# Kernel tuning notes

Hardware: AMD Instinct MI355X
Metric: run time of the kernel (lower is better)

Reference implementation:

```python
import jax, jax.numpy as jnp
import numpy as np

ALPHA = 32.0 ** 2
HEADS = 8
DIM_HEAD = 64
EPS = 1e-5


def _leaky(x):
    return jnp.where(x >= 0, x, 0.1 * x)


def _cpb_bias(fmap_size, w0, b0, w1, b1, w2, b2):
    # continuous position bias: MLP over signed-log relative coords -> [h, n, n]
    pos = jnp.arange(fmap_size)
    gi, gj = jnp.meshgrid(pos, pos, indexing='ij')
    grid = jnp.stack([gi, gj], axis=-1).reshape(-1, 2)  # [n, 2]
    rel = grid[:, None, :] - grid[None, :, :]           # [n, n, 2]
    rel = jnp.sign(rel) * jnp.log(jnp.abs(rel) + 1.0)
    h = _leaky(jnp.einsum('ijc,dc->ijd', rel.astype(jnp.float32), w0) + b0)
    h = _leaky(jnp.einsum('ijc,dc->ijd', h, w1) + b1)
    h = jnp.einsum('ijc,hc->ijh', h, w2) + b2           # [n, n, heads]
    return jnp.transpose(h, (2, 0, 1))                  # [heads, n, n]


def _stable_softmax(t, alpha=ALPHA):
    t = t / alpha
    t = t - jax.lax.stop_gradient(jnp.max(t, axis=-1, keepdims=True))
    return jax.nn.softmax(t * alpha, axis=-1)


def setup_inputs() -> dict:
    key = jax.random.key(0)
    ks = jax.random.split(key, 9)
    B, C, H, W = 8, 512, 32, 32
    inner = HEADS * DIM_HEAD
    s = 0.05
    return {
        'x': jax.random.normal(ks[0], (B, C, H, W), jnp.float32),
        'gamma': jnp.ones((1, C, 1, 1), jnp.float32),
        'w_qkv': jax.random.normal(ks[1], (inner * 3, C), jnp.float32) * s,
        'w_out': jax.random.normal(ks[2], (C, inner), jnp.float32) * s,
        'cpb_w0': jax.random.normal(ks[3], (128, 2), jnp.float32) * s,
        'cpb_b0': jax.random.normal(ks[4], (128,), jnp.float32) * s,
        'cpb_w1': jax.random.normal(ks[5], (128, 128), jnp.float32) * s,
        'cpb_b1': jax.random.normal(ks[6], (128,), jnp.float32) * s,
        'cpb_w2': jax.random.normal(ks[7], (HEADS, 128), jnp.float32) * s,
        'cpb_b2': jax.random.normal(ks[8], (HEADS,), jnp.float32) * s,
    }


def reference(x, gamma, w_qkv, w_out, cpb_w0, cpb_b0, cpb_w1, cpb_b1, cpb_w2, cpb_b2):
    B, C, H, W = x.shape
    n = H * W
    scale = DIM_HEAD ** -0.5
    residual = x

    # LayerNormChan: normalize over channel dim with biased variance
    mean = jnp.mean(x, axis=1, keepdims=True)
    var = jnp.var(x, axis=1, keepdims=True)
    xn = (x - mean) / jnp.sqrt(var + EPS) * gamma

    # 1x1 conv qkv projection as matmul over channels
    xf = xn.reshape(B, C, n)                              # [B, C, n]
    qkv = jnp.einsum('oc,bcn->bon', w_qkv, xf)            # [B, 3*inner, n]
    q, k, v = jnp.split(qkv, 3, axis=1)
    rs = lambda t: t.reshape(B, HEADS, DIM_HEAD, n)
    q, k, v = rs(q), rs(k), rs(v)

    sim = jnp.einsum('bhdi,bhdj->bhij', q, k) * scale     # [B, h, n, n]
    bias = _cpb_bias(H, cpb_w0, cpb_b0, cpb_w1, cpb_b1, cpb_w2, cpb_b2)
    sim = sim + bias[None]

    attn = _stable_softmax(sim)
    out = jnp.einsum('bhij,bhdj->bhdi', attn, v)          # [B, h, d, n]
    out = out.reshape(B, HEADS * DIM_HEAD, n)
    out = jnp.einsum('oc,bcn->bon', w_out, out).reshape(B, C, H, W)
    return out + residual
```

## Files before the change

kernel.cpp:

```cpp
#include <hip/hip_runtime.h>
#include <hip/hip_bf16.h>

#define CCH   512
#define BATCH 8
#define NPOS  1024
#define MQKV  1536
#define EPS   1e-5f
#define LOG2E 1.4426950408889634f

typedef __attribute__((ext_vector_type(4))) float f32x4;
typedef __attribute__((ext_vector_type(8))) __bf16 bf16x8;
typedef __attribute__((ext_vector_type(8))) unsigned short u16x8;
typedef __attribute__((ext_vector_type(4))) unsigned short u16x4;

__device__ inline unsigned short f2bf(float f) {
  __hip_bfloat16 h = __float2bfloat16(f);
  return __builtin_bit_cast(unsigned short, h);
}
__device__ inline float bf2f(unsigned short u) {
  return __bfloat162float(__builtin_bit_cast(__hip_bfloat16, u));
}

__device__ inline int sw(int row, int col) { return row * 64 + (col ^ ((row & 7) << 3)); }
__device__ inline int swk(int row, int col) { return row * 64 + (col ^ (((row >> 2) & 7) << 3)); }
__device__ inline int sw32(int row, int lh) {
  return row * 32 + ((lh ^ ((row ^ (row >> 2)) & 3)) << 3);
}

__device__ inline void gload16(const void* g, void* l) {
  __builtin_amdgcn_global_load_lds((const __attribute__((address_space(1))) void*)g,
                                   (__attribute__((address_space(3))) void*)l, 16, 0, 0);
}

#define CBAR(N) do {                                              \
    asm volatile("s_waitcnt vmcnt(" #N ")" ::: "memory");         \
    asm volatile("s_waitcnt lgkmcnt(0)" ::: "memory");            \
    __builtin_amdgcn_s_barrier();                                 \
  } while (0)

__global__ __launch_bounds__(256) void setup_kernel(
    const float* __restrict__ wq, const float* __restrict__ wo,
    unsigned short* __restrict__ wqb, unsigned short* __restrict__ wob,
    const float* __restrict__ x, const float* __restrict__ gamma,
    unsigned short* __restrict__ xnT,
    const float* __restrict__ table, unsigned short* __restrict__ biasP) {
  __shared__ float red[4][32][2];
  __shared__ float gsh[512];
  __shared__ unsigned short obuf[32 * 520];
  int bid = blockIdx.x, tid = threadIdx.x;

  if (bid >= 640) {
    int base = ((bid - 640) * 256 + tid) * 8;
    int h = base >> 20;
    int i = (base >> 10) & 1023;
    int j0 = base & 1023;
    int ib = i >> 5, il = i & 31;
    u16x8 outv;
    #pragma unroll
    for (int e = 0; e < 8; ++e) {
      int j = j0 + e;
      int dy = ib - (j >> 5) + 31;
      int dx = il - (j & 31) + 31;
      outv[e] = f2bf(table[h * 3969 + dy * 63 + dx]);
    }
    *(u16x8*)&biasP[base] = outv;
    return;
  }

  if (bid < 384) {
    int base = bid * 2048 + tid * 8;
    float sc = (base < 512 * CCH) ? (0.125f * LOG2E) : 1.0f;
    f32x4 v0 = *(const f32x4*)&wq[base];
    f32x4 v1 = *(const f32x4*)&wq[base + 4];
    u16x8 outv;
    #pragma unroll
    for (int e = 0; e < 4; ++e) outv[e] = f2bf(v0[e] * sc);
    #pragma unroll
    for (int e = 0; e < 4; ++e) outv[4 + e] = f2bf(v1[e] * sc);
    *(u16x8*)&wqb[base] = outv;
    if (base < CCH * CCH) {
      f32x4 w0v = *(const f32x4*)&wo[base];
      f32x4 w1v = *(const f32x4*)&wo[base + 4];
      u16x8 ov;
      #pragma unroll
      for (int e = 0; e < 4; ++e) ov[e] = f2bf(w0v[e]);
      #pragma unroll
      for (int e = 0; e < 4; ++e) ov[4 + e] = f2bf(w1v[e]);
      *(u16x8*)&wob[base] = ov;
    }
  } else {
    int blk = bid - 384;
    int b = blk >> 5, p0 = (blk & 31) * 32;
    int pl = tid & 31, wv = tid >> 6, cg = tid >> 5;
    gsh[tid] = gamma[tid];
    gsh[tid + 256] = gamma[tid + 256];
    const float* xp = x + (size_t)b * CCH * NPOS + p0 + pl;
    float vals[64];
    float s1 = 0.f, s2 = 0.f;
    #pragma unroll
    for (int j = 0; j < 64; ++j) {
      float v = xp[(size_t)(cg + 8 * j) * NPOS];
      vals[j] = v; s1 += v; s2 += v * v;
    }
    s1 += __shfl_xor(s1, 32, 64); s2 += __shfl_xor(s2, 32, 64);
    if ((tid & 63) < 32) { red[wv][pl][0] = s1; red[wv][pl][1] = s2; }
    __syncthreads();
    float t1 = 0.f, t2 = 0.f;
    #pragma unroll
    for (int w2i = 0; w2i < 4; ++w2i) { t1 += red[w2i][pl][0]; t2 += red[w2i][pl][1]; }
    float mean = t1 * (1.f / 512.f);
    float var = t2 * (1.f / 512.f) - mean * mean;
    float rstd = rsqrtf(var + EPS);
    #pragma unroll
    for (int j = 0; j < 64; ++j) {
      int c = cg + 8 * j;
      obuf[pl * 520 + c] = f2bf((vals[j] - mean) * rstd * gsh[c]);
    }
    __syncthreads();
    unsigned short* orow = xnT + ((size_t)b * NPOS + p0) * 512;
    #pragma unroll
    for (int i = 0; i < 8; ++i) {
      int c2 = tid + i * 256;
      int pp = c2 >> 6, ch = c2 & 63;
      *(u16x8*)&orow[(size_t)pp * 512 + ch * 8] = *(const u16x8*)&obuf[pp * 520 + ch * 8];
    }
  }
}

__global__ __launch_bounds__(256) void cpb_kernel(
    const float* __restrict__ w0, const float* __restrict__ b0,
    const float* __restrict__ w1, const float* __restrict__ b1,
    const float* __restrict__ w2, const float* __restrict__ b2,
    float* __restrict__ table) {
  __shared__ float w1s[128 * 129];
  __shared__ float w2s[8 * 128];
  __shared__ float sh1[2][128];
  __shared__ float sh2[2][128];
  int tid = threadIdx.x;
  #pragma unroll
  for (int i = 0; i < 64; ++i) {
    int idx = i * 256 + tid;
    w1s[(idx >> 7) * 129 + (idx & 127)] = w1[idx];
  }
  #pragma unroll
  for (int i = 0; i < 4; ++i) {
    int idx = i * 256 + tid;
    w2s[idx] = w2[idx];
  }
  int sub = tid >> 7, t = tid & 127;
  float w00 = w0[t * 2 + 0], w01 = w0[t * 2 + 1], bb0 = b0[t], bb1 = b1[t];
  int hh = t >> 4, k16 = t & 15;
  float b2h = b2[hh];
  __syncthreads();

  #pragma unroll 1
  for (int pass = 0; pass < 8; ++pass) {
    int d0 = (blockIdx.x * 8 + pass) * 2 + sub;
    bool ok = d0 < 3969;
    int d0c = ok ? d0 : 0;
    int dy = d0c / 63 - 31, dx = d0c % 63 - 31;
    float r0 = (dy > 0 ? 1.f : (dy < 0 ? -1.f : 0.f)) * logf(fabsf((float)dy) + 1.f);
    float r1 = (dx > 0 ? 1.f : (dx < 0 ? -1.f : 0.f)) * logf(fabsf((float)dx) + 1.f);
    float h0 = r0 * w00 + r1 * w01 + bb0;
    sh1[sub][t] = (h0 >= 0.f) ? h0 : 0.1f * h0;
    __syncthreads();
    float a = bb1;
    #pragma unroll 8
    for (int c = 0; c < 128; ++c) a += sh1[sub][c] * w1s[t * 129 + c];
    sh2[sub][t] = (a >= 0.f) ? a : 0.1f * a;
    __syncthreads();
    float o = 0.f;
    #pragma unroll
    for (int c = 0; c < 8; ++c) o += sh2[sub][k16 * 8 + c] * w2s[hh * 128 + k16 * 8 + c];
    #pragma unroll
    for (int mm = 1; mm < 16; mm <<= 1) o += __shfl_xor(o, mm, 64);
    if (k16 == 0 && ok) table[hh * 3969 + d0] = (o + b2h) * LOG2E;
    __syncthreads();
  }
}

__global__ __launch_bounds__(256) void gemm_qkv(const unsigned short* __restrict__ Ag,
                                                const unsigned short* __restrict__ Bg,
                                                unsigned short* __restrict__ qT,
                                                unsigned short* __restrict__ kT,
                                                unsigned short* __restrict__ vB) {
  __shared__ unsigned short smem[24576];
  int tid = threadIdx.x;
  int by = blockIdx.y;
  int m0 = by * 128, nn0 = blockIdx.x * 128;
  int wave = tid >> 6, lane = tid & 63;
  int wm = wave >> 1, wn = wave & 1;
  int l16 = lane & 15, lh = lane >> 4;
  int r4 = lane >> 2, c4 = lane & 3;
  int csw = ((c4 ^ (r4 & 3) ^ ((lane >> 4) & 3))) << 3;
  f32x4 acc[4][4];
  #pragma unroll
  for (int it = 0; it < 4; ++it)
    #pragma unroll
    for (int jt = 0; jt < 4; ++jt) acc[it][jt] = (f32x4){0.f, 0.f, 0.f, 0.f};

  #define GSTAGE(bsel, k0) do {                                                               \
    _Pragma("unroll")                                                                         \
    for (int i_ = 0; i_ < 2; ++i_) {                                                          \
      int grp_ = wave * 2 + i_;                                                               \
      int row_ = grp_ * 16 + r4;                                                              \
      gload16(&Ag[(size_t)(m0 + row_) * 512 + (k0) + csw], smem + (bsel) * 4096 + grp_ * 512);\
      gload16(&Bg[(size_t)(nn0 + row_) * 512 + (k0) + csw],                                   \
              smem + 12288 + (bsel) * 4096 + grp_ * 512);                                     \
    }                                                                                         \
  } while (0)

  GSTAGE(0, 0);
  GSTAGE(1, 32);
  asm volatile("s_waitcnt vmcnt(4)" ::: "memory");
  __builtin_amdgcn_s_barrier();
  int cur = 0;
  #pragma unroll 1
  for (int k = 0; k < 16; ++k) {
    int stg = (cur == 0) ? 2 : cur - 1;
    if (k < 14) GSTAGE(stg, (k + 2) * 32);
    const unsigned short* As = smem + cur * 4096;
    const unsigned short* Bs = smem + 12288 + cur * 4096;
    bf16x8 a[4], b[4];
    #pragma unroll
    for (int it = 0; it < 4; ++it) a[it] = *(const bf16x8*)&As[sw32(wm * 64 + it * 16 + l16, lh)];
    #pragma unroll
    for (int jt = 0; jt < 4; ++jt) b[jt] = *(const bf16x8*)&Bs[sw32(wn * 64 + jt * 16 + l16, lh)];
    __builtin_amdgcn_s_setprio(1);
    #pragma unroll
    for (int it = 0; it < 4; ++it)
      #pragma unroll
      for (int jt = 0; jt < 4; ++jt)
        acc[it][jt] = __builtin_amdgcn_mfma_f32_16x16x32_bf16(a[it], b[jt], acc[it][jt], 0, 0, 0);
    __builtin_amdgcn_s_setprio(0);
    if (k < 14) CBAR(4); else CBAR(0);
    cur = (cur == 2) ? 0 : cur + 1;
  }

  int sel = by >> 2;
  int hh0 = (by & 3) * 2;
  int bb = nn0 >> 10, p0 = nn0 & 1023;
  unsigned short* Cs = smem;
  if (sel < 2) {
    #pragma unroll
    for (int it = 0; it < 4; ++it)
      #pragma unroll
      for (int jt = 0; jt < 4; ++jt) {
        int nnl = wn * 64 + jt * 16 + l16;
        int mb = wm * 64 + it * 16 + lh * 4;
        #pragma unroll
        for (int r = 0; r < 4; ++r)
          Cs[nnl * 128 + ((mb + r) ^ ((nnl & 7) << 4))] = f2bf(acc[it][jt][r]);
      }
    __syncthreads();
    unsigned short* dst = (sel == 0) ? qT : kT;
    #pragma unroll
    for (int i = 0; i < 8; ++i) {
      int c = tid + i * 256;
      int hl = c >> 10, p = (c >> 3) & 127, ch = c & 7;
      int mb = hl * 64 + ch * 8;
      u16x8 val = *(u16x8*)&Cs[p * 128 + (mb ^ ((p & 7) << 4))];
      int bh = bb * 8 + hh0 + hl;
      *(u16x8*)&dst[((size_t)bh * 1024 + p0 + p) * 64 + ch * 8] = val;
    }
  } else {
    #pragma unroll
    for (int it = 0; it < 4; ++it)
      #pragma unroll
      for (int jt = 0; jt < 4; ++jt) {
        int nnl = wn * 64 + jt * 16 + l16;
        int mb = wm * 64 + it * 16 + lh * 4;
        #pragma unroll
        for (int r = 0; r < 4; ++r)
          Cs[(mb + r) * 128 + (nnl ^ (((mb + r) & 7) << 4))] = f2bf(acc[it][jt][r]);
      }
    __syncthreads();
    #pragma unroll
    for (int i = 0; i < 8; ++i) {
      int c = tid + i * 256;
      int mloc = c >> 4, ch = c & 15;
      u16x8 val = *(u16x8*)&Cs[mloc * 128 + ((ch * 8) ^ ((mloc & 7) << 4))];
      int d = mloc & 63, hl = mloc >> 6;
      int bh = bb * 8 + hh0 + hl;
      *(u16x8*)&vB[((size_t)bh * 64 + d) * 1024 + p0 + ch * 8] = val;
    }
  }
}

__global__ __launch_bounds__(256) void gemm_out(const unsigned short* __restrict__ Ag,
                                                const unsigned short* __restrict__ Bg,
                                                const float* __restrict__ xres,
                                                float* __restrict__ yout) {
  __shared__ unsigned short smem[18432];
  int tid = threadIdx.x;
  int m0 = blockIdx.y * 64, nn0 = blockIdx.x * 128;
  int wave = tid >> 6, lane = tid & 63;
  int wm = wave >> 1, wn = wave & 1;
  int l16 = lane & 15, lh = lane >> 4;
  int r4 = lane >> 2, c4 = lane & 3;
  int csw = ((c4 ^ (r4 & 3) ^ ((lane >> 4) & 3))) << 3;
  f32x4 acc[2][4];
  #pragma unroll
  for (int it = 0; it < 2; ++it)
    #pragma unroll
    for (int jt = 0; jt < 4; ++jt) acc[it][jt] = (f32x4){0.f, 0.f, 0.f, 0.f};

  #define OSTAGE(bsel, k0) do {                                                               \
    {                                                                                         \
      int row_ = wave * 16 + r4;                                                              \
      gload16(&Ag[(size_t)(m0 + row_) * 512 + (k0) + csw],                                    \
              smem + (bsel) * 2048 + wave * 512);                                             \
    }                                                                                         \
    _Pragma("unroll")                                                                         \
    for (int i_ = 0; i_ < 2; ++i_) {                                                          \
      int grp_ = wave * 2 + i_;                                                               \
      int row_ = grp_ * 16 + r4;                                                              \
      gload16(&Bg[(size_t)(nn0 + row_) * 512 + (k0) + csw],                                   \
              smem + 6144 + (bsel) * 4096 + grp_ * 512);                                      \
    }                                                                                         \
  } while (0)

  OSTAGE(0, 0);
  OSTAGE(1, 32);
  asm volatile("s_waitcnt vmcnt(3)" ::: "memory");
  __builtin_amdgcn_s_barrier();
  int cur = 0;
  #pragma unroll 1
  for (int k = 0; k < 16; ++k) {
    int stg = (cur == 0) ? 2 : cur - 1;
    if (k < 14) OSTAGE(stg, (k + 2) * 32);
    const unsigned short* As = smem + cur * 2048;
    const unsigned short* Bs = smem + 6144 + cur * 4096;
    bf16x8 a[2], b[4];
    #pragma unroll
    for (int it = 0; it < 2; ++it) a[it] = *(const bf16x8*)&As[sw32(wm * 32 + it * 16 + l16, lh)];
    #pragma unroll
    for (int jt = 0; jt < 4; ++jt) b[jt] = *(const bf16x8*)&Bs[sw32(wn * 64 + jt * 16 + l16, lh)];
    __builtin_amdgcn_s_setprio(1);
    #pragma unroll
    for (int it = 0; it < 2; ++it)
      #pragma unroll
      for (int jt = 0; jt < 4; ++jt)
        acc[it][jt] = __builtin_amdgcn_mfma_f32_16x16x32_bf16(a[it], b[jt], acc[it][jt], 0, 0, 0);
    __builtin_amdgcn_s_setprio(0);
    if (k < 14) CBAR(3); else CBAR(0);
    cur = (cur == 2) ? 0 : cur + 1;
  }

  #pragma unroll
  for (int it = 0; it < 2; ++it) {
    int mbase = m0 + wm * 32 + it * 16 + lh * 4;
    #pragma unroll
    for (int jt = 0; jt < 4; ++jt) {
      int nn = nn0 + wn * 64 + jt * 16 + l16;
      int bb = nn >> 10, p = nn & 1023;
      #pragma unroll
      for (int r = 0; r < 4; ++r) {
        size_t addr = ((size_t)bb * 512 + mbase + r) * 1024 + p;
        yout[addr] = acc[it][jt][r] + xres[addr];
      }
    }
  }
}

__global__ __launch_bounds__(512) void attn_kernel(const unsigned short* __restrict__ qT,
                                                   const unsigned short* __restrict__ kT,
                                                   const unsigned short* __restrict__ vB,
                                                   const unsigned short* __restrict__ biasP,
                                                   unsigned short* __restrict__ attnout) {
  __shared__ unsigned short Kbuf[3][64 * 64];
  __shared__ unsigned short Vbuf[3][64 * 64];
  __shared__ unsigned short Ps[8][16 * 64];
  int tid = threadIdx.x;
  int bh = blockIdx.x;
  int i0 = blockIdx.y * 128;
  int hh = bh & 7, bb = bh >> 3;
  int w = tid >> 6, lane = tid & 63, l16 = lane & 15, lh = lane >> 4;
  int rsub = lane >> 3, csub = lane & 7;
  int scswV = (csub ^ rsub) * 8;
  int scswK = (csub ^ ((w * 2 + (rsub >> 2)) & 7)) * 8;

  const unsigned short* kbase = kT + (size_t)bh * NPOS * 64;
  const unsigned short* vbase = vB + (size_t)bh * 64 * NPOS;
  const unsigned short* bptr  = biasP + ((size_t)hh * 1024 + i0 + w * 16) * 1024 + l16 * 4;

  int qrow = i0 + w * 16 + l16;
  const unsigned short* qb = qT + ((size_t)bh * NPOS + qrow) * 64 + lh * 8;
  bf16x8 qreg[2];
  qreg[0] = *(const bf16x8*)&qb[0];
  qreg[1] = *(const bf16x8*)&qb[32];

  f32x4 o[5];
  #pragma unroll
  for (int dt = 0; dt < 5; ++dt) o[dt] = (f32x4){0.f, 0.f, 0.f, 0.f};

  bf16x8 ones;
  {
    u16x8 tmp = {0x3F80, 0x3F80, 0x3F80, 0x3F80, 0x3F80, 0x3F80, 0x3F80, 0x3F80};
    ones = __builtin_bit_cast(bf16x8, tmp);
  }

  #define STAGE(Kd, Vd, jj) do {                                                        \
    gload16(&kbase[(size_t)((jj) + w * 8 + rsub) * 64 + scswK], &(Kd)[w * 512]);        \
    gload16(&vbase[(size_t)(w * 8 + rsub) * 1024 + (jj) + scswV], &(Vd)[w * 512]);      \
  } while (0)

  STAGE(Kbuf[0], Vbuf[0], 0);
  u16x4 bvc[4];
  #pragma unroll
  for (int r = 0; r < 4; ++r) bvc[r] = *(const u16x4*)&bptr[(lh * 4 + r) * 1024];
  STAGE(Kbuf[1], Vbuf[1], 64);
  asm volatile("s_waitcnt vmcnt(6)" ::: "memory");
  __builtin_amdgcn_s_barrier();
  int cur = 0;

  #pragma unroll 1
  for (int t = 0; t < 16; ++t) {
    int j0 = t * 64;

    u16x4 bvn[4];
    if (t < 15) {
      #pragma unroll
      for (int r = 0; r < 4; ++r) bvn[r] = *(const u16x4*)&bptr[(lh * 4 + r) * 1024 + j0 + 64];
    }

    int stg = (cur == 0) ? 2 : cur - 1;
    if (t < 14) STAGE(Kbuf[stg], Vbuf[stg], j0 + 128);

    const unsigned short* Ks = Kbuf[cur];
    const unsigned short* Vs = Vbuf[cur];

    f32x4 s[4];
    #pragma unroll
    for (int jt = 0; jt < 4; ++jt) s[jt] = (f32x4){0.f, 0.f, 0.f, 0.f};
    __builtin_amdgcn_s_setprio(1);
    #pragma unroll
    for (int ks = 0; ks < 2; ++ks) {
      int koff = ks * 32 + lh * 8;
      #pragma unroll
      for (int jt = 0; jt < 4; ++jt) {
        bf16x8 bk = *(const bf16x8*)&Ks[swk(l16 * 4 + jt, koff)];
        s[jt] = __builtin_amdgcn_mfma_f32_16x16x32_bf16(qreg[ks], bk, s[jt], 0, 0, 0);
      }
    }
    __builtin_amdgcn_s_setprio(0);

    #pragma unroll
    for (int r = 0; r < 4; ++r) {
      int rloc = lh * 4 + r;
      u16x4 pq;
      #pragma unroll
      for (int jt = 0; jt < 4; ++jt)
        pq[jt] = f2bf(__builtin_amdgcn_exp2f(s[jt][r] + bf2f(bvc[r][jt])));
      *(u16x4*)&Ps[w][sw(rloc, l16 * 4)] = pq;
    }

    __builtin_amdgcn_s_setprio(1);
    #pragma unroll
    for (int js = 0; js < 2; ++js) {
      int koff = js * 32 + lh * 8;
      bf16x8 pa = *(const bf16x8*)&Ps[w][sw(l16, koff)];
      #pragma unroll
      for (int dt = 0; dt < 4; ++dt) {
        bf16x8 vb = *(const bf16x8*)&Vs[sw(dt * 16 + l16, koff)];
        o[dt] = __builtin_amdgcn_mfma_f32_16x16x32_bf16(pa, vb, o[dt], 0, 0, 0);
      }
      o[4] = __builtin_amdgcn_mfma_f32_16x16x32_bf16(pa, ones, o[4], 0, 0, 0);
    }
    __builtin_amdgcn_s_setprio(0);

    if (t < 15) {
      #pragma unroll
      for (int r = 0; r < 4; ++r) bvc[r] = bvn[r];
    }

    if (t < 14) CBAR(6);
    else if (t == 14) CBAR(4);
    else CBAR(0);
    cur = (cur == 2) ? 0 : cur + 1;
  }

  #pragma unroll
  for (int r = 0; r < 4; ++r) {
    float inv = 1.f / o[4][r];
    int gi = i0 + w * 16 + lh * 4 + r;
    #pragma unroll
    for (int dt = 0; dt < 4; ++dt)
      attnout[((size_t)bb * 1024 + gi) * 512 + hh * 64 + dt * 16 + l16] = f2bf(o[dt][r] * inv);
  }
}

extern "C" void kernel_launch(void* const* d_in, const int* in_sizes, int n_in,
                              void* d_out, int out_size, void* d_ws, size_t ws_size,
                              hipStream_t stream) {
  const float* x     = (const float*)d_in[0];
  const float* gamma = (const float*)d_in[1];
  const float* w_qkv = (const float*)d_in[2];
  const float* w_out = (const float*)d_in[3];
  const float* cw0   = (const float*)d_in[4];
  const float* cb0   = (const float*)d_in[5];
  const float* cw1   = (const float*)d_in[6];
  const float* cb1   = (const float*)d_in[7];
  const float* cw2   = (const float*)d_in[8];
  const float* cb2   = (const float*)d_in[9];
  float* out = (float*)d_out;

  char* ws = (char*)d_ws;
  unsigned short* xnT   = (unsigned short*)(ws + 0);
  unsigned short* wqb   = (unsigned short*)(ws + 8388608);
  unsigned short* wob   = (unsigned short*)(ws + 9961472);
  unsigned short* qT    = (unsigned short*)(ws + 10485760);
  unsigned short* kT    = (unsigned short*)(ws + 18874368);
  unsigned short* vB    = (unsigned short*)(ws + 27262976);
  float*          table = (float*)(ws + 35651584);
  unsigned short* biasP = (unsigned short*)(ws + 35782656);
  unsigned short* aout  = (unsigned short*)(ws + 52559872);

  cpb_kernel<<<256, 256, 0, stream>>>(cw0, cb0, cw1, cb1, cw2, cb2, table);
  setup_kernel<<<4736, 256, 0, stream>>>(w_qkv, w_out, wqb, wob, x, gamma, xnT, table, biasP);
  gemm_qkv<<<dim3(64, 12), 256, 0, stream>>>(wqb, xnT, qT, kT, vB);
  attn_kernel<<<dim3(64, 8), 512, 0, stream>>>(qT, kT, vB, biasP, aout);
  gemm_out<<<dim3(64, 8), 256, 0, stream>>>(wob, aout, x, out);
}
```

Before: 99.39 us.

## Use 32x32x16 MFMA in attention with 4 waves of 32 query rows each

The attention kernel moves from 8 waves each handling 16 query rows with 16x16x32 MFMAs to 4 waves each handling 32 rows with 32x32x16 MFMAs. QK^T is computed transposed (K as the A operand), and P, V and the denominator use the larger tiles. The block shrinks to 256 threads, so each wave issues twice the K/V staging loads, and the bias load and output write patterns change. The aim is higher MFMA efficiency and fewer LDS reads per FLOP, at the cost of more registers per wave and fewer waves to hide latency.

```diff
diff --git a/kernel.cpp b/kernel.cpp
--- a/kernel.cpp
+++ b/kernel.cpp
@@ -9,6 +9,7 @@
 #define LOG2E 1.4426950408889634f
 
 typedef __attribute__((ext_vector_type(4))) float f32x4;
+typedef __attribute__((ext_vector_type(16))) float f32x16;
 typedef __attribute__((ext_vector_type(8))) __bf16 bf16x8;
 typedef __attribute__((ext_vector_type(8))) unsigned short u16x8;
 typedef __attribute__((ext_vector_type(4))) unsigned short u16x4;
@@ -22,7 +23,6 @@
 }
 
 __device__ inline int sw(int row, int col) { return row * 64 + (col ^ ((row & 7) << 3)); }
-__device__ inline int swk(int row, int col) { return row * 64 + (col ^ (((row >> 2) & 7) << 3)); }
 __device__ inline int sw32(int row, int lh) {
   return row * 32 + ((lh ^ ((row ^ (row >> 2)) & 3)) << 3);
 }
@@ -363,36 +363,36 @@
   }
 }
 
-__global__ __launch_bounds__(512) void attn_kernel(const unsigned short* __restrict__ qT,
+__global__ __launch_bounds__(256) void attn_kernel(const unsigned short* __restrict__ qT,
                                                    const unsigned short* __restrict__ kT,
                                                    const unsigned short* __restrict__ vB,
                                                    const unsigned short* __restrict__ biasP,
                                                    unsigned short* __restrict__ attnout) {
   __shared__ unsigned short Kbuf[3][64 * 64];
   __shared__ unsigned short Vbuf[3][64 * 64];
-  __shared__ unsigned short Ps[8][16 * 64];
+  __shared__ unsigned short Ps[4][32 * 64];
   int tid = threadIdx.x;
   int bh = blockIdx.x;
   int i0 = blockIdx.y * 128;
   int hh = bh & 7, bb = bh >> 3;
-  int w = tid >> 6, lane = tid & 63, l16 = lane & 15, lh = lane >> 4;
+  int w = tid >> 6, lane = tid & 63;
+  int l32 = lane & 31, hi = lane >> 5;
   int rsub = lane >> 3, csub = lane & 7;
-  int scswV = (csub ^ rsub) * 8;
-  int scswK = (csub ^ ((w * 2 + (rsub >> 2)) & 7)) * 8;
+  int scsw = (csub ^ rsub) * 8;
 
   const unsigned short* kbase = kT + (size_t)bh * NPOS * 64;
   const unsigned short* vbase = vB + (size_t)bh * 64 * NPOS;
-  const unsigned short* bptr  = biasP + ((size_t)hh * 1024 + i0 + w * 16) * 1024 + l16 * 4;
-
-  int qrow = i0 + w * 16 + l16;
-  const unsigned short* qb = qT + ((size_t)bh * NPOS + qrow) * 64 + lh * 8;
-  bf16x8 qreg[2];
-  qreg[0] = *(const bf16x8*)&qb[0];
-  qreg[1] = *(const bf16x8*)&qb[32];
-
-  f32x4 o[5];
-  #pragma unroll
-  for (int dt = 0; dt < 5; ++dt) o[dt] = (f32x4){0.f, 0.f, 0.f, 0.f};
+  int qg = i0 + w * 32 + l32;
+  const unsigned short* bptr = biasP + ((size_t)hh * 1024 + qg) * 1024;
+
+  const unsigned short* qb = qT + ((size_t)bh * NPOS + qg) * 64;
+  bf16x8 qreg[4];
+  #pragma unroll
+  for (int s = 0; s < 4; ++s) qreg[s] = *(const bf16x8*)&qb[s * 16 + hi * 8];
+
+  f32x16 acc[2], den;
+  #pragma unroll
+  for (int e = 0; e < 16; ++e) { acc[0][e] = 0.f; acc[1][e] = 0.f; den[e] = 0.f; }
 
   bf16x8 ones;
   {
@@ -400,17 +400,28 @@
     ones = __builtin_bit_cast(bf16x8, tmp);
   }
 
-  #define STAGE(Kd, Vd, jj) do {                                                        \
-    gload16(&kbase[(size_t)((jj) + w * 8 + rsub) * 64 + scswK], &(Kd)[w * 512]);        \
-    gload16(&vbase[(size_t)(w * 8 + rsub) * 1024 + (jj) + scswV], &(Vd)[w * 512]);      \
+  #define STAGE(Kd, Vd, jj) do {                                                          \
+    _Pragma("unroll")                                                                     \
+    for (int i_ = 0; i_ < 2; ++i_) {                                                      \
+      int grp_ = w * 2 + i_;                                                              \
+      gload16(&kbase[(size_t)((jj) + grp_ * 8 + rsub) * 64 + scsw], &(Kd)[grp_ * 512]);   \
+      gload16(&vbase[(size_t)(grp_ * 8 + rsub) * 1024 + (jj) + scsw], &(Vd)[grp_ * 512]); \
+    }                                                                                     \
   } while (0)
 
+  #define BLOAD(dst, jj) do {                                                             \
+    _Pragma("unroll")                                                                     \
+    for (int js_ = 0; js_ < 2; ++js_)                                                     \
+      _Pragma("unroll")                                                                   \
+      for (int m_ = 0; m_ < 4; ++m_)                                                      \
+        dst[js_ * 4 + m_] = *(const u16x4*)&bptr[(jj) + js_ * 32 + 4 * hi + 8 * m_];      \
+  } while (0)
+
   STAGE(Kbuf[0], Vbuf[0], 0);
-  u16x4 bvc[4];
-  #pragma unroll
-  for (int r = 0; r < 4; ++r) bvc[r] = *(const u16x4*)&bptr[(lh * 4 + r) * 1024];
+  u16x4 bvc[8];
+  BLOAD(bvc, 0);
   STAGE(Kbuf[1], Vbuf[1], 64);
-  asm volatile("s_waitcnt vmcnt(6)" ::: "memory");
+  asm volatile("s_waitcnt vmcnt(12)" ::: "memory");
   __builtin_amdgcn_s_barrier();
   int cur = 0;
 
@@ -418,11 +429,8 @@
   for (int t = 0; t < 16; ++t) {
     int j0 = t * 64;
 
-    u16x4 bvn[4];
-    if (t < 15) {
-      #pragma unroll
-      for (int r = 0; r < 4; ++r) bvn[r] = *(const u16x4*)&bptr[(lh * 4 + r) * 1024 + j0 + 64];
-    }
+    u16x4 bvn[8];
+    if (t < 15) BLOAD(bvn, j0 + 64);
 
     int stg = (cur == 0) ? 2 : cur - 1;
     if (t < 14) STAGE(Kbuf[stg], Vbuf[stg], j0 + 128);
@@ -430,63 +438,60 @@
     const unsigned short* Ks = Kbuf[cur];
     const unsigned short* Vs = Vbuf[cur];
 
-    f32x4 s[4];
-    #pragma unroll
-    for (int jt = 0; jt < 4; ++jt) s[jt] = (f32x4){0.f, 0.f, 0.f, 0.f};
+    f32x16 sT[2];
+    #pragma unroll
+    for (int e = 0; e < 16; ++e) { sT[0][e] = 0.f; sT[1][e] = 0.f; }
     __builtin_amdgcn_s_setprio(1);
     #pragma unroll
-    for (int ks = 0; ks < 2; ++ks) {
-      int koff = ks * 32 + lh * 8;
-      #pragma unroll
-      for (int jt = 0; jt < 4; ++jt) {
-        bf16x8 bk = *(const bf16x8*)&Ks[swk(l16 * 4 + jt, koff)];
-        s[jt] = __builtin_amdgcn_mfma_f32_16x16x32_bf16(qreg[ks], bk, s[jt], 0, 0, 0);
+    for (int js = 0; js < 2; ++js)
+      #pragma unroll
+      for (int s = 0; s < 4; ++s) {
+        bf16x8 ak = *(const bf16x8*)&Ks[sw(js * 32 + l32, s * 16 + hi * 8)];
+        sT[js] = __builtin_amdgcn_mfma_f32_32x32x16_bf16(ak, qreg[s], sT[js], 0, 0, 0);
       }
-    }
     __builtin_amdgcn_s_setprio(0);
 
     #pragma unroll
-    for (int r = 0; r < 4; ++r) {
-      int rloc = lh * 4 + r;
-      u16x4 pq;
-      #pragma unroll
-      for (int jt = 0; jt < 4; ++jt)
-        pq[jt] = f2bf(__builtin_amdgcn_exp2f(s[jt][r] + bf2f(bvc[r][jt])));
-      *(u16x4*)&Ps[w][sw(rloc, l16 * 4)] = pq;
-    }
+    for (int js = 0; js < 2; ++js)
+      #pragma unroll
+      for (int m = 0; m < 4; ++m) {
+        u16x4 pq;
+        #pragma unroll
+        for (int r = 0; r < 4; ++r)
+          pq[r] = f2bf(__builtin_amdgcn_exp2f(sT[js][m * 4 + r] + bf2f(bvc[js * 4 + m][r])));
+        *(u16x4*)&Ps[w][sw(l32, js * 32 + 4 * hi + 8 * m)] = pq;
+      }
 
     __builtin_amdgcn_s_setprio(1);
     #pragma unroll
-    for (int js = 0; js < 2; ++js) {
-      int koff = js * 32 + lh * 8;
-      bf16x8 pa = *(const bf16x8*)&Ps[w][sw(l16, koff)];
-      #pragma unroll
-      for (int dt = 0; dt < 4; ++dt) {
-        bf16x8 vb = *(const bf16x8*)&Vs[sw(dt * 16 + l16, koff)];
-        o[dt] = __builtin_amdgcn_mfma_f32_16x16x32_bf16(pa, vb, o[dt], 0, 0, 0);
+    for (int s = 0; s < 4; ++s) {
+      bf16x8 pa = *(const bf16x8*)&Ps[w][sw(l32, s * 16 + hi * 8)];
+      #pragma unroll
+      for (int dt = 0; dt < 2; ++dt) {
+        bf16x8 vb = *(const bf16x8*)&Vs[sw(dt * 32 + l32, s * 16 + hi * 8)];
+        acc[dt] = __builtin_amdgcn_mfma_f32_32x32x16_bf16(pa, vb, acc[dt], 0, 0, 0);
       }
-      o[4] = __builtin_amdgcn_mfma_f32_16x16x32_bf16(pa, ones, o[4], 0, 0, 0);
+      den = __builtin_amdgcn_mfma_f32_32x32x16_bf16(pa, ones, den, 0, 0, 0);
     }
     __builtin_amdgcn_s_setprio(0);
 
     if (t < 15) {
       #pragma unroll
-      for (int r = 0; r < 4; ++r) bvc[r] = bvn[r];
-    }
-
-    if (t < 14) CBAR(6);
-    else if (t == 14) CBAR(4);
-    else CBAR(0);
+      for (int b_ = 0; b_ < 8; ++b_) bvc[b_] = bvn[b_];
+    }
+
+    if (t < 14) CBAR(4); else CBAR(0);
     cur = (cur == 2) ? 0 : cur + 1;
   }
 
   #pragma unroll
-  for (int r = 0; r < 4; ++r) {
-    float inv = 1.f / o[4][r];
-    int gi = i0 + w * 16 + lh * 4 + r;
-    #pragma unroll
-    for (int dt = 0; dt < 4; ++dt)
-      attnout[((size_t)bb * 1024 + gi) * 512 + hh * 64 + dt * 16 + l16] = f2bf(o[dt][r] * inv);
+  for (int reg = 0; reg < 16; ++reg) {
+    int qrow = (reg & 3) + 8 * (reg >> 2) + 4 * hi;
+    int gi = i0 + w * 32 + qrow;
+    float inv = 1.f / den[reg];
+    unsigned short* orow = attnout + ((size_t)bb * 1024 + gi) * 512 + hh * 64 + l32;
+    orow[0]  = f2bf(acc[0][reg] * inv);
+    orow[32] = f2bf(acc[1][reg] * inv);
   }
 }
 
@@ -519,6 +524,6 @@
   cpb_kernel<<<256, 256, 0, stream>>>(cw0, cb0, cw1, cb1, cw2, cb2, table);
   setup_kernel<<<4736, 256, 0, stream>>>(w_qkv, w_out, wqb, wob, x, gamma, xnT, table, biasP);
   gemm_qkv<<<dim3(64, 12), 256, 0, stream>>>(wqb, xnT, qT, kT, vB);
-  attn_kernel<<<dim3(64, 8), 512, 0, stream>>>(qT, kT, vB, biasP, aout);
+  attn_kernel<<<dim3(64, 8), 256, 0, stream>>>(qT, kT, vB, biasP, aout);
   gemm_out<<<dim3(64, 8), 256, 0, stream>>>(wob, aout, x, out);
 }
```

New measurement: 112.1 us. 1.13x slower.
